# Performance work log

Hardware: AMD Instinct MI355X
Metric: run time of the kernel (lower is better)

The kernel has to match this reference:

```python
import jax, jax.numpy as jnp
import numpy as np

H, I, C, B, T = 128, 270, 3, 1024, 270


def setup_inputs() -> dict:
    key = jax.random.key(0)
    ks = jax.random.split(key, 6)
    inp = {
        "x": jax.random.normal(ks[0], (B, T, I), dtype=jnp.float32),
        "Wf": jax.random.normal(ks[1], (H, I + H), dtype=jnp.float32) * 0.01,
        "Wi": jax.random.normal(ks[2], (H, I + H), dtype=jnp.float32) * 0.01,
        "Wc": jax.random.normal(ks[3], (H, I + H), dtype=jnp.float32) * 0.01,
        "Wo": jax.random.normal(ks[4], (H, I + H), dtype=jnp.float32) * 0.01,
        "Wy": jax.random.normal(ks[5], (C, H), dtype=jnp.float32) * 0.01,
        "bf": jnp.zeros((H,), jnp.float32),
        "bi": jnp.zeros((H,), jnp.float32),
        "bc": jnp.zeros((H,), jnp.float32),
        "bo": jnp.zeros((H,), jnp.float32),
        "by": jnp.zeros((C,), jnp.float32),
    }
    return inp


def _lstm_forward(x, Wf, Wi, Wc, Wo, Wy, bf, bi, bc, bo, by):
    # combined = [h_prev, x_t], so W[:, :H] acts on h, W[:, H:] acts on x.
    Wh = jnp.stack([Wf[:, :H], Wi[:, :H], Wc[:, :H], Wo[:, :H]])      # [4,H,H]
    Wx = jnp.stack([Wf[:, H:], Wi[:, H:], Wc[:, H:], Wo[:, H:]])      # [4,H,I]
    b = jnp.stack([bf, bi, bc, bo])                                   # [4,H]
    # Precompute input projections for all timesteps: one big GEMM.
    xp = jnp.einsum('bti,ghi->tbgh', x, Wx)                           # [T,B,4,H]

    def step(carry, xpt):
        h, c = carry
        pre = xpt + jnp.einsum('bh,gkh->bgk', h, Wh) + b              # [B,4,H]
        f = jax.nn.sigmoid(pre[:, 0])
        i = jax.nn.sigmoid(pre[:, 1])
        g = jnp.tanh(pre[:, 2])
        o = jax.nn.sigmoid(pre[:, 3])
        c_new = f * c + i * g
        h_new = o * jnp.tanh(c_new)
        return (h_new, c_new), h_new

    h0 = jnp.zeros((x.shape[0], H), x.dtype)
    c0 = jnp.zeros((x.shape[0], H), x.dtype)
    _, hs = jax.lax.scan(step, (h0, c0), xp)                          # hs: [T,B,H]
    all_hiddens = jnp.transpose(hs, (1, 0, 2))                        # [B,T,H]
    logits = jnp.einsum('bth,ch->btc', all_hiddens, Wy) + by
    all_outputs = jax.nn.softmax(logits, axis=-1)                     # [B,T,C]
    return all_hiddens, all_outputs


def reference(x, Wf, Wi, Wc, Wo, Wy, bf, bi, bc, bo, by):
    return _lstm_forward(x, Wf, Wi, Wc, Wo, Wy, bf, bi, bc, bo, by)
```

## Files before the change

### kernel.cpp

```cpp
#include <hip/hip_runtime.h>
#include <stdint.h>


typedef __attribute__((ext_vector_type(8))) short short8;
typedef __attribute__((ext_vector_type(4))) float f32x4;
typedef __attribute__((ext_vector_type(2))) float f32x2;
typedef __attribute__((ext_vector_type(4))) unsigned int uint4v;
typedef __attribute__((ext_vector_type(2))) unsigned int u32x2;
typedef unsigned short ush;

__device__ __forceinline__ ush f2bf(float f) {
    unsigned u = __float_as_uint(f);
    return (ush)((u + 0x7FFFu + ((u >> 16) & 1u)) >> 16);
}
__device__ __forceinline__ float bf2f(ush s) { return __uint_as_float(((unsigned)s) << 16); }
__device__ __forceinline__ float sigm_f(float x) {
    x = fminf(fmaxf(x, -30.f), 30.f);
    return __builtin_amdgcn_rcpf(1.f + __expf(-x));
}
__device__ __forceinline__ float tanh_f(float x) {
    x = fminf(fmaxf(x, -15.f), 15.f);
    float e = __expf(-2.f * x);
    return (1.f - e) * __builtin_amdgcn_rcpf(1.f + e);
}
__device__ __forceinline__ void lds_barrier() {
    asm volatile("s_waitcnt lgkmcnt(0)" ::: "memory");
    __builtin_amdgcn_s_barrier();
    __builtin_amdgcn_sched_barrier(0);
    asm volatile("" ::: "memory");
}

__global__ __launch_bounds__(256) void pack_w(
    const float* __restrict__ Wf, const float* __restrict__ Wi,
    const float* __restrict__ Wc, const float* __restrict__ Wo,
    const float* __restrict__ bf_, const float* __restrict__ bi_,
    const float* __restrict__ bc_, const float* __restrict__ bo_,
    ush* __restrict__ Wxp, ush* __restrict__ Whp, float* __restrict__ bpk)
{
    int idx = blockIdx.x * 256 + threadIdx.x;
    if (idx < 512 * 288) {
        int u = idx / 288, i = idx - u * 288;
        int g = u >> 7, j = u & 127;
        const float* Wg = (g == 0) ? Wf : (g == 1) ? Wi : (g == 2) ? Wc : Wo;
        float v = (i < 270) ? Wg[(size_t)j * 398 + 128 + i] : 0.f;
        Wxp[idx] = f2bf(v);
    }
    if (idx < 512 * 128) {
        int u = idx >> 7, k = idx & 127;
        int g = u >> 7, j = u & 127;
        const float* Wg = (g == 0) ? Wf : (g == 1) ? Wi : (g == 2) ? Wc : Wo;
        Whp[idx] = f2bf(Wg[(size_t)j * 398 + k]);
    }
    if (idx < 512) {
        int g = idx >> 7, j = idx & 127;
        const float* bg = (g == 0) ? bf_ : (g == 1) ? bi_ : (g == 2) ? bc_ : bo_;
        bpk[idx] = bg[j];
    }
}

__global__ __launch_bounds__(256, 2) void xp_gemm(
    const float* __restrict__ x, const ush* __restrict__ Wxp,
    const float* __restrict__ bpk, ush* __restrict__ xpc, int t0)
{
    __shared__ ush A_lds[64 * 296];
    const int tid = threadIdx.x;
    const int l = tid & 63, w = tid >> 6;
    const int l16 = l & 15, lq = l >> 4;
    const size_t row0 = (size_t)blockIdx.x * 64;

    const int srow = tid >> 2, sgrp = tid & 3;
    const int r = (int)row0 + srow;
    const int b = r & 1023, tt = (r >> 10) + t0;
    const float* xrow = x + ((size_t)b * 270 + tt) * 270;
    f32x2 stg[9][4];
    #pragma unroll
    for (int ks = 0; ks < 9; ++ks) {
        const int col = ks * 32 + sgrp * 8;
        const float* p = xrow + col;
        if (col + 8 <= 270) {
            stg[ks][0] = *(const f32x2*)p;       stg[ks][1] = *(const f32x2*)(p + 2);
            stg[ks][2] = *(const f32x2*)(p + 4); stg[ks][3] = *(const f32x2*)(p + 6);
        } else {
            float tv[8];
            #pragma unroll
            for (int j = 0; j < 8; ++j) tv[j] = (col + j < 270) ? p[j] : 0.f;
            stg[ks][0] = (f32x2){tv[0], tv[1]}; stg[ks][1] = (f32x2){tv[2], tv[3]};
            stg[ks][2] = (f32x2){tv[4], tv[5]}; stg[ks][3] = (f32x2){tv[6], tv[7]};
        }
    }

    const ush* bptr = Wxp + ((size_t)(w * 128 + l16)) * 288 + lq * 8;
    short8 bA[8], bB[8];
    #pragma unroll
    for (int nt = 0; nt < 8; ++nt) bA[nt] = *(const short8*)(bptr + nt * 4608);
    float bias_v[8];
    #pragma unroll
    for (int nt = 0; nt < 8; ++nt) bias_v[nt] = bpk[w * 128 + nt * 16 + l16];

    {
        ush* wrow = &A_lds[srow * 296 + sgrp * 8];
        #pragma unroll
        for (int ks = 0; ks < 9; ++ks) {
            uint4v o;
            #pragma unroll
            for (int p2 = 0; p2 < 4; ++p2) {
                unsigned v;
                asm("v_cvt_pk_bf16_f32 %0, %1, %2"
                    : "=v"(v) : "v"(stg[ks][p2].x), "v"(stg[ks][p2].y));
                o[p2] = v;
            }
            *(uint4v*)(wrow + ks * 32) = o;
        }
    }
    lds_barrier();

    f32x4 acc[4][8];
    #pragma unroll
    for (int mt = 0; mt < 4; ++mt)
        #pragma unroll
        for (int nt = 0; nt < 8; ++nt)
            acc[mt][nt] = (f32x4){bias_v[nt], bias_v[nt], bias_v[nt], bias_v[nt]};

    #pragma unroll
    for (int ks = 0; ks < 9; ++ks) {
        short8* cur = (ks & 1) ? bB : bA;
        short8* nxt = (ks & 1) ? bA : bB;
        if (ks + 1 < 9) {
            const ush* np = bptr + (ks + 1) * 32;
            #pragma unroll
            for (int nt = 0; nt < 8; ++nt) nxt[nt] = *(const short8*)(np + nt * 4608);
        }
        short8 afr[4];
        #pragma unroll
        for (int mt = 0; mt < 4; ++mt)
            afr[mt] = *(const short8*)(&A_lds[(mt * 16 + l16) * 296 + ks * 32 + lq * 8]);
        #pragma unroll
        for (int mt = 0; mt < 4; ++mt)
            #pragma unroll
            for (int nt = 0; nt < 8; ++nt)
                acc[mt][nt] = __builtin_amdgcn_mfma_f32_16x16x32_bf16(
                    afr[mt], cur[nt], acc[mt][nt], 0, 0, 0);
    }

    const int tloc = (int)(row0 >> 10);
    const int bg0 = ((int)row0 & 1023) >> 4;
    #pragma unroll
    for (int mt = 0; mt < 4; ++mt)
        #pragma unroll
        for (int nt = 0; nt < 8; ++nt) {
            int u = w * 128 + nt * 16 + l16;
            ush* dst = xpc + ((size_t)(tloc * 64 + bg0 + mt) * 512 + u) * 16 + lq * 4;
            #pragma unroll
            for (int q = 0; q < 4; ++q) dst[q] = f2bf(acc[mt][nt][q]);
        }
}

#define STEPB(T, PS)                                                            \
  {                                                                             \
    const int t_ = (T);                                                         \
    short8 afr[4];                                                              \
    _Pragma("unroll") for (int kf = 0; kf < 4; ++kf) {                          \
      int off_ = ((l16 * 128 + kf * 32 + lq * 8) * 2) ^ ((l16 & 7) << 4);       \
      afr[kf] = *(const short8*)((const char*)&h_lds[0][0] + cur * 4096 + off_);\
    }                                                                           \
    f32x4 a0_[4], a1_[4];                                                       \
    _Pragma("unroll") for (int g = 0; g < 4; ++g) {                             \
      a0_[g] = (f32x4){0.f, 0.f, 0.f, 0.f};                                     \
      a1_[g] = (f32x4){0.f, 0.f, 0.f, 0.f};                                     \
    }                                                                           \
    _Pragma("unroll") for (int g = 0; g < 4; ++g) {                             \
      a0_[g] = __builtin_amdgcn_mfma_f32_16x16x32_bf16(afr[0], whf[g][0], a0_[g], 0, 0, 0); \
      a1_[g] = __builtin_amdgcn_mfma_f32_16x16x32_bf16(afr[2], whf[g][2], a1_[g], 0, 0, 0); \
      a0_[g] = __builtin_amdgcn_mfma_f32_16x16x32_bf16(afr[1], whf[g][1], a0_[g], 0, 0, 0); \
      a1_[g] = __builtin_amdgcn_mfma_f32_16x16x32_bf16(afr[3], whf[g][3], a1_[g], 0, 0, 0); \
    }                                                                           \
    f32x4 ay_ = (f32x4){0.f, 0.f, 0.f, 0.f};                                    \
    if (w < 4 && t_ > t0) {               \
      ay_ = __builtin_amdgcn_mfma_f32_16x16x32_bf16(afr[0], wyf[0], ay_, 0, 0, 0); \
      ay_ = __builtin_amdgcn_mfma_f32_16x16x32_bf16(afr[1], wyf[1], ay_, 0, 0, 0); \
      ay_ = __builtin_amdgcn_mfma_f32_16x16x32_bf16(afr[2], wyf[2], ay_, 0, 0, 0); \
      ay_ = __builtin_amdgcn_mfma_f32_16x16x32_bf16(afr[3], wyf[3], ay_, 0, 0, 0); \
    }                                                                           \
    float xg_[4][4];                                                            \
    _Pragma("unroll") for (int g = 0; g < 4; ++g) {                             \
      u32x2 pv_ = PS[g];                                                        \
      xg_[g][0] = __uint_as_float(pv_.x << 16);                                 \
      xg_[g][1] = __uint_as_float(pv_.x & 0xffff0000u);                         \
      xg_[g][2] = __uint_as_float(pv_.y << 16);                                 \
      xg_[g][3] = __uint_as_float(pv_.y & 0xffff0000u);                         \
    }                                                                           \
    if (t_ + 2 < t1) {                                                          \
      const ush* pn_ = xb + (size_t)(t_ + 2 - t0) * TSTEP;                      \
      _Pragma("unroll") for (int g = 0; g < 4; ++g)                             \
        PS[g] = *(const u32x2*)(pn_ + go[g]);                                   \
    }                                                                           \
    float hv_[4];                                                               \
    _Pragma("unroll") for (int q = 0; q < 4; ++q) {                             \
      float pf_ = a0_[0][q] + a1_[0][q] + xg_[0][q];                            \
      float pi_ = a0_[1][q] + a1_[1][q] + xg_[1][q];                            \
      float pc_ = a0_[2][q] + a1_[2][q] + xg_[2][q];                            \
      float po_ = a0_[3][q] + a1_[3][q] + xg_[3][q];                            \
      float fg_ = sigm_f(pf_);                                                  \
      float ig_ = sigm_f(pi_);                                                  \
      float gg_ = tanh_f(pc_);                                                  \
      float og_ = sigm_f(po_);                                                  \
      float cn_ = fg_ * c[q] + ig_ * gg_;                                       \
      c[q] = cn_;                                                               \
      hv_[q] = og_ * tanh_f(cn_);                                               \
    }                                                                           \
    _Pragma("unroll") for (int q = 0; q < 4; ++q) {                             \
      int rr_ = lq * 4 + q;                                                     \
      int off_ = ((rr_ * 128 + jcol) * 2) ^ ((rr_ & 7) << 4);                   \
      *(ush*)((char*)&h_lds[0][0] + (cur ^ 1) * 4096 + off_) = f2bf(hv_[q]);    \
      out0[(size_t)(b0 + rr_) * (270 * 128) + (size_t)t_ * 128 + jcol] = hv_[q];\
    }                                                                           \
    if (w < 4 && t_ > t0) {                                                     \
      float L_ = ((w == 0) ? ay_[0] : (w == 1) ? ay_[1] : (w == 2) ? ay_[2] : ay_[3]) + byl; \
      if (l16 >= 3) L_ = -1e30f;                                                \
      float m_ = fmaxf(L_, __shfl_xor(L_, 1));                                  \
      m_ = fmaxf(m_, __shfl_xor(m_, 2));                                        \
      float e_ = (l16 < 3) ? __expf(L_ - m_) : 0.f;                             \
      float s_ = e_ + __shfl_xor(e_, 1);                                        \
      s_ = s_ + __shfl_xor(s_, 2);                                              \
      if (l16 < 3)                                                              \
        out1[((size_t)(b0 + lq * 4 + w) * 270 + (t_ - 1)) * 3 + l16] = e_ * __builtin_amdgcn_rcpf(s_); \
    }                                                                           \
    lds_barrier();                                                              \
    cur ^= 1;                                                                   \
  }

__global__ __launch_bounds__(512) void lstm_scan(
    const ush* __restrict__ xpc, const ush* __restrict__ Whp,
    float* __restrict__ c_state, float* __restrict__ out0, float* __restrict__ out1,
    const float* __restrict__ Wy, const float* __restrict__ by, int t0, int t1)
{
    __shared__ ush h_lds[2][16 * 128];
    const int tid = threadIdx.x;
    const int l = tid & 63, w = tid >> 6;
    const int l16 = l & 15, lq = l >> 4;
    const int b0 = blockIdx.x * 16;
    const int jcol = w * 16 + l16;

    short8 whf[4][4];
    #pragma unroll
    for (int g = 0; g < 4; ++g) {
        const ush* bw = Whp + ((size_t)(g * 128 + jcol)) * 128 + lq * 8;
        #pragma unroll
        for (int kf = 0; kf < 4; ++kf) whf[g][kf] = *(const short8*)(bw + kf * 32);
    }
    short8 wyf[4];
    #pragma unroll
    for (int kf = 0; kf < 4; ++kf) {
        short8 fr;
        #pragma unroll
        for (int j = 0; j < 8; ++j)
            fr[j] = (l16 < 3) ? (short)f2bf(Wy[l16 * 128 + kf * 32 + lq * 8 + j]) : (short)0;
        wyf[kf] = fr;
    }
    const float byl = (l16 < 3) ? by[l16] : 0.f;

    {
        ush* hp = &h_lds[0][0];
        for (int idx = tid; idx < 2 * 16 * 128; idx += 512) hp[idx] = 0;
    }
    __syncthreads();

    int cur = 0;
    float c[4] = {0.f, 0.f, 0.f, 0.f};
    if (t0 != 0) {
        #pragma unroll
        for (int q = 0; q < 4; ++q)
            c[q] = c_state[(size_t)(b0 + lq * 4 + q) * 128 + jcol];
        for (int idx = tid; idx < 2048; idx += 512) {
            int rr = idx >> 7, k = idx & 127;
            float hvv = out0[(size_t)(b0 + rr) * (270 * 128) + (size_t)(t0 - 1) * 128 + k];
            int off = ((rr * 128 + k) * 2) ^ ((rr & 7) << 4);
            *(ush*)((char*)&h_lds[0][0] + off) = f2bf(hvv);
        }
        __syncthreads();
    }

    const size_t TSTEP = (size_t)64 * 512 * 16;
    const ush* xb = xpc + (size_t)blockIdx.x * 8192;
    int go[4];
    #pragma unroll
    for (int g = 0; g < 4; ++g) go[g] = (g * 128 + jcol) * 16 + lq * 4;

    u32x2 Pa[4], Pb[4];
    #pragma unroll
    for (int g = 0; g < 4; ++g) Pa[g] = *(const u32x2*)(xb + go[g]);
    #pragma unroll
    for (int g = 0; g < 4; ++g) Pb[g] = *(const u32x2*)(xb + TSTEP + go[g]);

    for (int t = t0; t < t1; t += 2) {
        STEPB(t, Pa)
        STEPB(t + 1, Pb)
    }

    {
        short8 afr[4];
        #pragma unroll
        for (int kf = 0; kf < 4; ++kf) {
            int off = ((l16 * 128 + kf * 32 + lq * 8) * 2) ^ ((l16 & 7) << 4);
            afr[kf] = *(const short8*)((const char*)&h_lds[0][0] + cur * 4096 + off);
        }
        if (w < 4) {
            f32x4 ay = (f32x4){0.f, 0.f, 0.f, 0.f};
            ay = __builtin_amdgcn_mfma_f32_16x16x32_bf16(afr[0], wyf[0], ay, 0, 0, 0);
            ay = __builtin_amdgcn_mfma_f32_16x16x32_bf16(afr[1], wyf[1], ay, 0, 0, 0);
            ay = __builtin_amdgcn_mfma_f32_16x16x32_bf16(afr[2], wyf[2], ay, 0, 0, 0);
            ay = __builtin_amdgcn_mfma_f32_16x16x32_bf16(afr[3], wyf[3], ay, 0, 0, 0);
            float L = ((w == 0) ? ay[0] : (w == 1) ? ay[1] : (w == 2) ? ay[2] : ay[3]) + byl;
            if (l16 >= 3) L = -1e30f;
            float m = fmaxf(L, __shfl_xor(L, 1));
            m = fmaxf(m, __shfl_xor(m, 2));
            float e = (l16 < 3) ? __expf(L - m) : 0.f;
            float s = e + __shfl_xor(e, 1);
            s = s + __shfl_xor(s, 2);
            if (l16 < 3)
                out1[((size_t)(b0 + lq * 4 + w) * 270 + (t1 - 1)) * 3 + l16] =
                    e * __builtin_amdgcn_rcpf(s);
        }
    }

    if (t1 != 270) {
        #pragma unroll
        for (int q = 0; q < 4; ++q)
            c_state[(size_t)(b0 + lq * 4 + q) * 128 + jcol] = c[q];
    }
}

extern "C" void kernel_launch(void* const* d_in, const int* in_sizes, int n_in,
                              void* d_out, int out_size, void* d_ws, size_t ws_size,
                              hipStream_t stream) {
    (void)in_sizes; (void)n_in; (void)out_size;
    const float* x   = (const float*)d_in[0];
    const float* Wf  = (const float*)d_in[1];
    const float* Wi  = (const float*)d_in[2];
    const float* Wc  = (const float*)d_in[3];
    const float* Wo  = (const float*)d_in[4];
    const float* Wy  = (const float*)d_in[5];
    const float* bfp = (const float*)d_in[6];
    const float* bip = (const float*)d_in[7];
    const float* bcp = (const float*)d_in[8];
    const float* bop = (const float*)d_in[9];
    const float* byp = (const float*)d_in[10];

    float* out0 = (float*)d_out;
    float* out1 = out0 + (size_t)1024 * 270 * 128;

    long tc = 6;
    {
        const long cand[6] = {270, 90, 54, 30, 18, 6};
        for (int i = 0; i < 6; ++i) {
            size_t need = (size_t)cand[i] * 1048576u + (2u << 20);
            if (need <= ws_size) { tc = cand[i]; break; }
        }
    }
    char* wsb = (char*)d_ws;
    ush* xpc = (ush*)wsb;
    char* fx = wsb + (size_t)tc * 1048576u;
    float* c_state = (float*)fx;
    ush* Wxp = (ush*)(fx + 524288);
    ush* Whp = (ush*)(fx + 524288 + 294912);
    float* bpk = (float*)(fx + 524288 + 294912 + 131072);

    pack_w<<<576, 256, 0, stream>>>(Wf, Wi, Wc, Wo, bfp, bip, bcp, bop, Wxp, Whp, bpk);

    for (int t0 = 0; t0 < 270; t0 += (int)tc) {
        int Tcur = (270 - t0) < (int)tc ? (270 - t0) : (int)tc;
        int rows = Tcur * 1024;
        xp_gemm<<<rows / 64, 256, 0, stream>>>(x, Wxp, bpk, xpc, t0);
        lstm_scan<<<64, 512, 0, stream>>>(xpc, Whp, c_state, out0, out1, Wy, byp,
                                          t0, t0 + Tcur);
    }
}
```

Measured before the change: 501.5 us.

## Fuse input-projection GEMM and recurrent scan into one kernel with double-buffered chunks

Replaces the separate xp_gemm and lstm_scan launches with a single fused kernel. Blocks 0-63 run the recurrent scan on chunk ci-1 while blocks 64-255 compute the input projection for chunk ci into a second buffer, so the GEMM overlaps the latency-bound scan. The chunk size is capped at 54 timesteps. The x-projection is also folded into the MFMA accumulator init instead of being added after the matmuls. The cost is that the GEMM blocks now compete with the scan blocks for CU and memory resources, plus the overhead of more launches.

```diff
diff --git a/kernel.cpp b/kernel.cpp
--- a/kernel.cpp
+++ b/kernel.cpp
@@ -5,7 +5,6 @@
 typedef __attribute__((ext_vector_type(8))) short short8;
 typedef __attribute__((ext_vector_type(4))) float f32x4;
 typedef __attribute__((ext_vector_type(2))) float f32x2;
-typedef __attribute__((ext_vector_type(4))) unsigned int uint4v;
 typedef __attribute__((ext_vector_type(2))) unsigned int u32x2;
 typedef unsigned short ush;
 
@@ -58,128 +57,13 @@
     }
 }
 
-__global__ __launch_bounds__(256, 2) void xp_gemm(
-    const float* __restrict__ x, const ush* __restrict__ Wxp,
-    const float* __restrict__ bpk, ush* __restrict__ xpc, int t0)
-{
-    __shared__ ush A_lds[64 * 296];
-    const int tid = threadIdx.x;
-    const int l = tid & 63, w = tid >> 6;
-    const int l16 = l & 15, lq = l >> 4;
-    const size_t row0 = (size_t)blockIdx.x * 64;
-
-    const int srow = tid >> 2, sgrp = tid & 3;
-    const int r = (int)row0 + srow;
-    const int b = r & 1023, tt = (r >> 10) + t0;
-    const float* xrow = x + ((size_t)b * 270 + tt) * 270;
-    f32x2 stg[9][4];
-    #pragma unroll
-    for (int ks = 0; ks < 9; ++ks) {
-        const int col = ks * 32 + sgrp * 8;
-        const float* p = xrow + col;
-        if (col + 8 <= 270) {
-            stg[ks][0] = *(const f32x2*)p;       stg[ks][1] = *(const f32x2*)(p + 2);
-            stg[ks][2] = *(const f32x2*)(p + 4); stg[ks][3] = *(const f32x2*)(p + 6);
-        } else {
-            float tv[8];
-            #pragma unroll
-            for (int j = 0; j < 8; ++j) tv[j] = (col + j < 270) ? p[j] : 0.f;
-            stg[ks][0] = (f32x2){tv[0], tv[1]}; stg[ks][1] = (f32x2){tv[2], tv[3]};
-            stg[ks][2] = (f32x2){tv[4], tv[5]}; stg[ks][3] = (f32x2){tv[6], tv[7]};
-        }
-    }
-
-    const ush* bptr = Wxp + ((size_t)(w * 128 + l16)) * 288 + lq * 8;
-    short8 bA[8], bB[8];
-    #pragma unroll
-    for (int nt = 0; nt < 8; ++nt) bA[nt] = *(const short8*)(bptr + nt * 4608);
-    float bias_v[8];
-    #pragma unroll
-    for (int nt = 0; nt < 8; ++nt) bias_v[nt] = bpk[w * 128 + nt * 16 + l16];
-
-    {
-        ush* wrow = &A_lds[srow * 296 + sgrp * 8];
-        #pragma unroll
-        for (int ks = 0; ks < 9; ++ks) {
-            uint4v o;
-            #pragma unroll
-            for (int p2 = 0; p2 < 4; ++p2) {
-                unsigned v;
-                asm("v_cvt_pk_bf16_f32 %0, %1, %2"
-                    : "=v"(v) : "v"(stg[ks][p2].x), "v"(stg[ks][p2].y));
-                o[p2] = v;
-            }
-            *(uint4v*)(wrow + ks * 32) = o;
-        }
-    }
-    lds_barrier();
-
-    f32x4 acc[4][8];
-    #pragma unroll
-    for (int mt = 0; mt < 4; ++mt)
-        #pragma unroll
-        for (int nt = 0; nt < 8; ++nt)
-            acc[mt][nt] = (f32x4){bias_v[nt], bias_v[nt], bias_v[nt], bias_v[nt]};
-
-    #pragma unroll
-    for (int ks = 0; ks < 9; ++ks) {
-        short8* cur = (ks & 1) ? bB : bA;
-        short8* nxt = (ks & 1) ? bA : bB;
-        if (ks + 1 < 9) {
-            const ush* np = bptr + (ks + 1) * 32;
-            #pragma unroll
-            for (int nt = 0; nt < 8; ++nt) nxt[nt] = *(const short8*)(np + nt * 4608);
-        }
-        short8 afr[4];
-        #pragma unroll
-        for (int mt = 0; mt < 4; ++mt)
-            afr[mt] = *(const short8*)(&A_lds[(mt * 16 + l16) * 296 + ks * 32 + lq * 8]);
-        #pragma unroll
-        for (int mt = 0; mt < 4; ++mt)
-            #pragma unroll
-            for (int nt = 0; nt < 8; ++nt)
-                acc[mt][nt] = __builtin_amdgcn_mfma_f32_16x16x32_bf16(
-                    afr[mt], cur[nt], acc[mt][nt], 0, 0, 0);
-    }
-
-    const int tloc = (int)(row0 >> 10);
-    const int bg0 = ((int)row0 & 1023) >> 4;
-    #pragma unroll
-    for (int mt = 0; mt < 4; ++mt)
-        #pragma unroll
-        for (int nt = 0; nt < 8; ++nt) {
-            int u = w * 128 + nt * 16 + l16;
-            ush* dst = xpc + ((size_t)(tloc * 64 + bg0 + mt) * 512 + u) * 16 + lq * 4;
-            #pragma unroll
-            for (int q = 0; q < 4; ++q) dst[q] = f2bf(acc[mt][nt][q]);
-        }
-}
-
 #define STEPB(T, PS)                                                            \
   {                                                                             \
     const int t_ = (T);                                                         \
     short8 afr[4];                                                              \
     _Pragma("unroll") for (int kf = 0; kf < 4; ++kf) {                          \
       int off_ = ((l16 * 128 + kf * 32 + lq * 8) * 2) ^ ((l16 & 7) << 4);       \
-      afr[kf] = *(const short8*)((const char*)&h_lds[0][0] + cur * 4096 + off_);\
-    }                                                                           \
-    f32x4 a0_[4], a1_[4];                                                       \
-    _Pragma("unroll") for (int g = 0; g < 4; ++g) {                             \
-      a0_[g] = (f32x4){0.f, 0.f, 0.f, 0.f};                                     \
-      a1_[g] = (f32x4){0.f, 0.f, 0.f, 0.f};                                     \
-    }                                                                           \
-    _Pragma("unroll") for (int g = 0; g < 4; ++g) {                             \
-      a0_[g] = __builtin_amdgcn_mfma_f32_16x16x32_bf16(afr[0], whf[g][0], a0_[g], 0, 0, 0); \
-      a1_[g] = __builtin_amdgcn_mfma_f32_16x16x32_bf16(afr[2], whf[g][2], a1_[g], 0, 0, 0); \
-      a0_[g] = __builtin_amdgcn_mfma_f32_16x16x32_bf16(afr[1], whf[g][1], a0_[g], 0, 0, 0); \
-      a1_[g] = __builtin_amdgcn_mfma_f32_16x16x32_bf16(afr[3], whf[g][3], a1_[g], 0, 0, 0); \
-    }                                                                           \
-    f32x4 ay_ = (f32x4){0.f, 0.f, 0.f, 0.f};                                    \
-    if (w < 4 && t_ > t0) {               \
-      ay_ = __builtin_amdgcn_mfma_f32_16x16x32_bf16(afr[0], wyf[0], ay_, 0, 0, 0); \
-      ay_ = __builtin_amdgcn_mfma_f32_16x16x32_bf16(afr[1], wyf[1], ay_, 0, 0, 0); \
-      ay_ = __builtin_amdgcn_mfma_f32_16x16x32_bf16(afr[2], wyf[2], ay_, 0, 0, 0); \
-      ay_ = __builtin_amdgcn_mfma_f32_16x16x32_bf16(afr[3], wyf[3], ay_, 0, 0, 0); \
+      afr[kf] = *(const short8*)(hbase + cur * 4096 + off_);                    \
     }                                                                           \
     float xg_[4][4];                                                            \
     _Pragma("unroll") for (int g = 0; g < 4; ++g) {                             \
@@ -194,12 +78,30 @@
       _Pragma("unroll") for (int g = 0; g < 4; ++g)                             \
         PS[g] = *(const u32x2*)(pn_ + go[g]);                                   \
     }                                                                           \
+    f32x4 a0_[4], a1_[4];                                                       \
+    _Pragma("unroll") for (int g = 0; g < 4; ++g) {                             \
+      a0_[g] = (f32x4){xg_[g][0], xg_[g][1], xg_[g][2], xg_[g][3]};             \
+      a1_[g] = (f32x4){0.f, 0.f, 0.f, 0.f};                                     \
+    }                                                                           \
+    _Pragma("unroll") for (int g = 0; g < 4; ++g) {                             \
+      a0_[g] = __builtin_amdgcn_mfma_f32_16x16x32_bf16(afr[0], whf[g][0], a0_[g], 0, 0, 0); \
+      a1_[g] = __builtin_amdgcn_mfma_f32_16x16x32_bf16(afr[2], whf[g][2], a1_[g], 0, 0, 0); \
+      a0_[g] = __builtin_amdgcn_mfma_f32_16x16x32_bf16(afr[1], whf[g][1], a0_[g], 0, 0, 0); \
+      a1_[g] = __builtin_amdgcn_mfma_f32_16x16x32_bf16(afr[3], whf[g][3], a1_[g], 0, 0, 0); \
+    }                                                                           \
+    f32x4 ay_ = (f32x4){0.f, 0.f, 0.f, 0.f};                                    \
+    if (w < 4 && t_ > t0) {               \
+      ay_ = __builtin_amdgcn_mfma_f32_16x16x32_bf16(afr[0], wyf[0], ay_, 0, 0, 0); \
+      ay_ = __builtin_amdgcn_mfma_f32_16x16x32_bf16(afr[1], wyf[1], ay_, 0, 0, 0); \
+      ay_ = __builtin_amdgcn_mfma_f32_16x16x32_bf16(afr[2], wyf[2], ay_, 0, 0, 0); \
+      ay_ = __builtin_amdgcn_mfma_f32_16x16x32_bf16(afr[3], wyf[3], ay_, 0, 0, 0); \
+    }                                                                           \
     float hv_[4];                                                               \
     _Pragma("unroll") for (int q = 0; q < 4; ++q) {                             \
-      float pf_ = a0_[0][q] + a1_[0][q] + xg_[0][q];                            \
-      float pi_ = a0_[1][q] + a1_[1][q] + xg_[1][q];                            \
-      float pc_ = a0_[2][q] + a1_[2][q] + xg_[2][q];                            \
-      float po_ = a0_[3][q] + a1_[3][q] + xg_[3][q];                            \
+      float pf_ = a0_[0][q] + a1_[0][q];                                        \
+      float pi_ = a0_[1][q] + a1_[1][q];                                        \
+      float pc_ = a0_[2][q] + a1_[2][q];                                        \
+      float po_ = a0_[3][q] + a1_[3][q];                                        \
       float fg_ = sigm_f(pf_);                                                  \
       float ig_ = sigm_f(pi_);                                                  \
       float gg_ = tanh_f(pc_);                                                  \
@@ -211,7 +113,7 @@
     _Pragma("unroll") for (int q = 0; q < 4; ++q) {                             \
       int rr_ = lq * 4 + q;                                                     \
       int off_ = ((rr_ * 128 + jcol) * 2) ^ ((rr_ & 7) << 4);                   \
-      *(ush*)((char*)&h_lds[0][0] + (cur ^ 1) * 4096 + off_) = f2bf(hv_[q]);    \
+      *(ush*)(hbase + (cur ^ 1) * 4096 + off_) = f2bf(hv_[q]);                  \
       out0[(size_t)(b0 + rr_) * (270 * 128) + (size_t)t_ * 128 + jcol] = hv_[q];\
     }                                                                           \
     if (w < 4 && t_ > t0) {                                                     \
@@ -229,104 +131,195 @@
     cur ^= 1;                                                                   \
   }
 
-__global__ __launch_bounds__(512) void lstm_scan(
-    const ush* __restrict__ xpc, const ush* __restrict__ Whp,
+__global__ __launch_bounds__(512) void fused_step(
+    const float* __restrict__ x, const ush* __restrict__ Wxp,
+    const float* __restrict__ bpk, ush* __restrict__ xpo,
+    const ush* __restrict__ xpi, const ush* __restrict__ Whp,
     float* __restrict__ c_state, float* __restrict__ out0, float* __restrict__ out1,
-    const float* __restrict__ Wy, const float* __restrict__ by, int t0, int t1)
+    const float* __restrict__ Wy, const float* __restrict__ by,
+    int tg0, int grows, int t0, int t1)
 {
-    __shared__ ush h_lds[2][16 * 128];
+    __shared__ ush smem[64 * 296];
     const int tid = threadIdx.x;
     const int l = tid & 63, w = tid >> 6;
     const int l16 = l & 15, lq = l >> 4;
-    const int b0 = blockIdx.x * 16;
-    const int jcol = w * 16 + l16;
-
-    short8 whf[4][4];
+
+    if (blockIdx.x < 64) {
+        if (t1 <= t0) return;
+        char* hbase = (char*)smem;
+        const int b0 = blockIdx.x * 16;
+        const int jcol = w * 16 + l16;
+
+        short8 whf[4][4];
+        #pragma unroll
+        for (int g = 0; g < 4; ++g) {
+            const ush* bw = Whp + ((size_t)(g * 128 + jcol)) * 128 + lq * 8;
+            #pragma unroll
+            for (int kf = 0; kf < 4; ++kf) whf[g][kf] = *(const short8*)(bw + kf * 32);
+        }
+        short8 wyf[4];
+        #pragma unroll
+        for (int kf = 0; kf < 4; ++kf) {
+            short8 fr;
+            #pragma unroll
+            for (int j = 0; j < 8; ++j)
+                fr[j] = (l16 < 3) ? (short)f2bf(Wy[l16 * 128 + kf * 32 + lq * 8 + j]) : (short)0;
+            wyf[kf] = fr;
+        }
+        const float byl = (l16 < 3) ? by[l16] : 0.f;
+
+        for (int idx = tid; idx < 4096; idx += 512) smem[idx] = 0;
+        __syncthreads();
+
+        int cur = 0;
+        float c[4] = {0.f, 0.f, 0.f, 0.f};
+        if (t0 != 0) {
+            #pragma unroll
+            for (int q = 0; q < 4; ++q)
+                c[q] = c_state[(size_t)(b0 + lq * 4 + q) * 128 + jcol];
+            for (int idx = tid; idx < 2048; idx += 512) {
+                int rr = idx >> 7, k = idx & 127;
+                float hvv = out0[(size_t)(b0 + rr) * (270 * 128) + (size_t)(t0 - 1) * 128 + k];
+                int off = ((rr * 128 + k) * 2) ^ ((rr & 7) << 4);
+                *(ush*)(hbase + off) = f2bf(hvv);
+            }
+            __syncthreads();
+        }
+
+        const size_t TSTEP = (size_t)64 * 512 * 16;
+        const ush* xb = xpi + (size_t)blockIdx.x * 8192;
+        int go[4];
+        #pragma unroll
+        for (int g = 0; g < 4; ++g) go[g] = (g * 128 + jcol) * 16 + lq * 4;
+
+        u32x2 Pa[4], Pb[4];
+        #pragma unroll
+        for (int g = 0; g < 4; ++g) Pa[g] = *(const u32x2*)(xb + go[g]);
+        #pragma unroll
+        for (int g = 0; g < 4; ++g) Pb[g] = *(const u32x2*)(xb + TSTEP + go[g]);
+
+        for (int t = t0; t < t1; t += 2) {
+            STEPB(t, Pa)
+            STEPB(t + 1, Pb)
+        }
+
+        {
+            short8 afr[4];
+            #pragma unroll
+            for (int kf = 0; kf < 4; ++kf) {
+                int off = ((l16 * 128 + kf * 32 + lq * 8) * 2) ^ ((l16 & 7) << 4);
+                afr[kf] = *(const short8*)(hbase + cur * 4096 + off);
+            }
+            if (w < 4) {
+                f32x4 ay = (f32x4){0.f, 0.f, 0.f, 0.f};
+                ay = __builtin_amdgcn_mfma_f32_16x16x32_bf16(afr[0], wyf[0], ay, 0, 0, 0);
+                ay = __builtin_amdgcn_mfma_f32_16x16x32_bf16(afr[1], wyf[1], ay, 0, 0, 0);
+                ay = __builtin_amdgcn_mfma_f32_16x16x32_bf16(afr[2], wyf[2], ay, 0, 0, 0);
+                ay = __builtin_amdgcn_mfma_f32_16x16x32_bf16(afr[3], wyf[3], ay, 0, 0, 0);
+                float L = ((w == 0) ? ay[0] : (w == 1) ? ay[1] : (w == 2) ? ay[2] : ay[3]) + byl;
+                if (l16 >= 3) L = -1e30f;
+                float m = fmaxf(L, __shfl_xor(L, 1));
+                m = fmaxf(m, __shfl_xor(m, 2));
+                float e = (l16 < 3) ? __expf(L - m) : 0.f;
+                float s = e + __shfl_xor(e, 1);
+                s = s + __shfl_xor(s, 2);
+                if (l16 < 3)
+                    out1[((size_t)(b0 + lq * 4 + w) * 270 + (t1 - 1)) * 3 + l16] =
+                        e * __builtin_amdgcn_rcpf(s);
+            }
+        }
+        if (t1 != 270) {
+            #pragma unroll
+            for (int q = 0; q < 4; ++q)
+                c_state[(size_t)(b0 + lq * 4 + q) * 128 + jcol] = c[q];
+        }
+        return;
+    }
+
+    if (grows <= 0) return;
+    const int ntiles = grows >> 6;
+    const int wave_m = w >> 2, wave_n = w & 3;
+    const int srow = tid >> 3, cg = tid & 7;
+
+    const ush* bptr = Wxp + ((size_t)(wave_n * 128 + l16)) * 288 + lq * 8;
+    float bias_v[8];
     #pragma unroll
-    for (int g = 0; g < 4; ++g) {
-        const ush* bw = Whp + ((size_t)(g * 128 + jcol)) * 128 + lq * 8;
-        #pragma unroll
-        for (int kf = 0; kf < 4; ++kf) whf[g][kf] = *(const short8*)(bw + kf * 32);
-    }
-    short8 wyf[4];
-    #pragma unroll
-    for (int kf = 0; kf < 4; ++kf) {
-        short8 fr;
-        #pragma unroll
-        for (int j = 0; j < 8; ++j)
-            fr[j] = (l16 < 3) ? (short)f2bf(Wy[l16 * 128 + kf * 32 + lq * 8 + j]) : (short)0;
-        wyf[kf] = fr;
-    }
-    const float byl = (l16 < 3) ? by[l16] : 0.f;
-
-    {
-        ush* hp = &h_lds[0][0];
-        for (int idx = tid; idx < 2 * 16 * 128; idx += 512) hp[idx] = 0;
-    }
-    __syncthreads();
-
-    int cur = 0;
-    float c[4] = {0.f, 0.f, 0.f, 0.f};
-    if (t0 != 0) {
-        #pragma unroll
-        for (int q = 0; q < 4; ++q)
-            c[q] = c_state[(size_t)(b0 + lq * 4 + q) * 128 + jcol];
-        for (int idx = tid; idx < 2048; idx += 512) {
-            int rr = idx >> 7, k = idx & 127;
-            float hvv = out0[(size_t)(b0 + rr) * (270 * 128) + (size_t)(t0 - 1) * 128 + k];
-            int off = ((rr * 128 + k) * 2) ^ ((rr & 7) << 4);
-            *(ush*)((char*)&h_lds[0][0] + off) = f2bf(hvv);
-        }
-        __syncthreads();
-    }
-
-    const size_t TSTEP = (size_t)64 * 512 * 16;
-    const ush* xb = xpc + (size_t)blockIdx.x * 8192;
-    int go[4];
-    #pragma unroll
-    for (int g = 0; g < 4; ++g) go[g] = (g * 128 + jcol) * 16 + lq * 4;
-
-    u32x2 Pa[4], Pb[4];
-    #pragma unroll
-    for (int g = 0; g < 4; ++g) Pa[g] = *(const u32x2*)(xb + go[g]);
-    #pragma unroll
-    for (int g = 0; g < 4; ++g) Pb[g] = *(const u32x2*)(xb + TSTEP + go[g]);
-
-    for (int t = t0; t < t1; t += 2) {
-        STEPB(t, Pa)
-        STEPB(t + 1, Pb)
-    }
-
-    {
-        short8 afr[4];
-        #pragma unroll
-        for (int kf = 0; kf < 4; ++kf) {
-            int off = ((l16 * 128 + kf * 32 + lq * 8) * 2) ^ ((l16 & 7) << 4);
-            afr[kf] = *(const short8*)((const char*)&h_lds[0][0] + cur * 4096 + off);
-        }
-        if (w < 4) {
-            f32x4 ay = (f32x4){0.f, 0.f, 0.f, 0.f};
-            ay = __builtin_amdgcn_mfma_f32_16x16x32_bf16(afr[0], wyf[0], ay, 0, 0, 0);
-            ay = __builtin_amdgcn_mfma_f32_16x16x32_bf16(afr[1], wyf[1], ay, 0, 0, 0);
-            ay = __builtin_amdgcn_mfma_f32_16x16x32_bf16(afr[2], wyf[2], ay, 0, 0, 0);
-            ay = __builtin_amdgcn_mfma_f32_16x16x32_bf16(afr[3], wyf[3], ay, 0, 0, 0);
-            float L = ((w == 0) ? ay[0] : (w == 1) ? ay[1] : (w == 2) ? ay[2] : ay[3]) + byl;
-            if (l16 >= 3) L = -1e30f;
-            float m = fmaxf(L, __shfl_xor(L, 1));
-            m = fmaxf(m, __shfl_xor(m, 2));
-            float e = (l16 < 3) ? __expf(L - m) : 0.f;
-            float s = e + __shfl_xor(e, 1);
-            s = s + __shfl_xor(s, 2);
-            if (l16 < 3)
-                out1[((size_t)(b0 + lq * 4 + w) * 270 + (t1 - 1)) * 3 + l16] =
-                    e * __builtin_amdgcn_rcpf(s);
-        }
-    }
-
-    if (t1 != 270) {
-        #pragma unroll
-        for (int q = 0; q < 4; ++q)
-            c_state[(size_t)(b0 + lq * 4 + q) * 128 + jcol] = c[q];
+    for (int nt = 0; nt < 8; ++nt) bias_v[nt] = bpk[wave_n * 128 + nt * 16 + l16];
+
+    for (int tile = (int)blockIdx.x - 64; tile < ntiles; tile += 192) {
+        const int r = tile * 64 + srow;
+        const int b = r & 1023, tt = (r >> 10) + tg0;
+        const float* xrow = x + ((size_t)b * 270 + tt) * 270;
+        f32x4 stg[9];
+        #pragma unroll
+        for (int ks = 0; ks < 9; ++ks) {
+            const int col = ks * 32 + cg * 4;
+            if (ks < 8) {
+                stg[ks] = *(const f32x4*)(xrow + col);
+            } else {
+                float tv[4];
+                #pragma unroll
+                for (int j = 0; j < 4; ++j) tv[j] = (col + j < 270) ? xrow[col + j] : 0.f;
+                stg[8] = (f32x4){tv[0], tv[1], tv[2], tv[3]};
+            }
+        }
+        lds_barrier();
+        {
+            ush* wp = smem + srow * 296 + cg * 4;
+            #pragma unroll
+            for (int ks = 0; ks < 9; ++ks) {
+                unsigned v0, v1;
+                asm("v_cvt_pk_bf16_f32 %0, %1, %2" : "=v"(v0) : "v"(stg[ks].x), "v"(stg[ks].y));
+                asm("v_cvt_pk_bf16_f32 %0, %1, %2" : "=v"(v1) : "v"(stg[ks].z), "v"(stg[ks].w));
+                u32x2 pk; pk.x = v0; pk.y = v1;
+                *(u32x2*)(wp + ks * 32) = pk;
+            }
+        }
+        short8 bA[8], bB[8];
+        #pragma unroll
+        for (int nt = 0; nt < 8; ++nt) bA[nt] = *(const short8*)(bptr + nt * 4608);
+        lds_barrier();
+
+        f32x4 acc[2][8];
+        #pragma unroll
+        for (int mt = 0; mt < 2; ++mt)
+            #pragma unroll
+            for (int nt = 0; nt < 8; ++nt)
+                acc[mt][nt] = (f32x4){bias_v[nt], bias_v[nt], bias_v[nt], bias_v[nt]};
+
+        #pragma unroll
+        for (int ks = 0; ks < 9; ++ks) {
+            short8* curb = (ks & 1) ? bB : bA;
+            short8* nxtb = (ks & 1) ? bA : bB;
+            if (ks + 1 < 9) {
+                const ush* np = bptr + (ks + 1) * 32;
+                #pragma unroll
+                for (int nt = 0; nt < 8; ++nt) nxtb[nt] = *(const short8*)(np + nt * 4608);
+            }
+            short8 afr[2];
+            #pragma unroll
+            for (int mt = 0; mt < 2; ++mt)
+                afr[mt] = *(const short8*)(&smem[(wave_m * 32 + mt * 16 + l16) * 296 + ks * 32 + lq * 8]);
+            #pragma unroll
+            for (int mt = 0; mt < 2; ++mt)
+                #pragma unroll
+                for (int nt = 0; nt < 8; ++nt)
+                    acc[mt][nt] = __builtin_amdgcn_mfma_f32_16x16x32_bf16(
+                        afr[mt], curb[nt], acc[mt][nt], 0, 0, 0);
+        }
+
+        const int tloc = (tile * 64) >> 10;
+        const int bgrp0 = ((tile * 64) & 1023) >> 4;
+        #pragma unroll
+        for (int mt = 0; mt < 2; ++mt)
+            #pragma unroll
+            for (int nt = 0; nt < 8; ++nt) {
+                const int bgrp = bgrp0 + wave_m * 2 + mt;
+                const int u = wave_n * 128 + nt * 16 + l16;
+                ush* dst = xpo + ((size_t)(tloc * 64 + bgrp) * 512 + u) * 16 + lq * 4;
+                #pragma unroll
+                for (int q = 0; q < 4; ++q) dst[q] = f2bf(acc[mt][nt][q]);
+            }
     }
 }
 
@@ -351,15 +344,17 @@
 
     long tc = 6;
     {
-        const long cand[6] = {270, 90, 54, 30, 18, 6};
-        for (int i = 0; i < 6; ++i) {
-            size_t need = (size_t)cand[i] * 1048576u + (2u << 20);
+        const long cand[4] = {54, 30, 18, 6};
+        for (int i = 0; i < 4; ++i) {
+            size_t need = (size_t)cand[i] * 2097152u + (2u << 20);
             if (need <= ws_size) { tc = cand[i]; break; }
         }
     }
+    const int nch = (int)(270 / tc);
     char* wsb = (char*)d_ws;
-    ush* xpc = (ush*)wsb;
-    char* fx = wsb + (size_t)tc * 1048576u;
+    ush* xpcA = (ush*)wsb;
+    ush* xpcB = (ush*)(wsb + (size_t)tc * 1048576u);
+    char* fx = wsb + (size_t)tc * 2097152u;
     float* c_state = (float*)fx;
     ush* Wxp = (ush*)(fx + 524288);
     ush* Whp = (ush*)(fx + 524288 + 294912);
@@ -367,11 +362,15 @@
 
     pack_w<<<576, 256, 0, stream>>>(Wf, Wi, Wc, Wo, bfp, bip, bcp, bop, Wxp, Whp, bpk);
 
-    for (int t0 = 0; t0 < 270; t0 += (int)tc) {
-        int Tcur = (270 - t0) < (int)tc ? (270 - t0) : (int)tc;
-        int rows = Tcur * 1024;
-        xp_gemm<<<rows / 64, 256, 0, stream>>>(x, Wxp, bpk, xpc, t0);
-        lstm_scan<<<64, 512, 0, stream>>>(xpc, Whp, c_state, out0, out1, Wy, byp,
-                                          t0, t0 + Tcur);
-    }
-}
+    for (int ci = 0; ci <= nch; ++ci) {
+        int g_t0 = ci * (int)tc;
+        int g_rows = (ci < nch) ? (int)tc * 1024 : 0;
+        int s_t0 = (ci > 0) ? (ci - 1) * (int)tc : 0;
+        int s_t1 = (ci > 0) ? ci * (int)tc : 0;
+        ush* xo = (ci & 1) ? xpcB : xpcA;
+        ush* xi = (ci & 1) ? xpcA : xpcB;
+        fused_step<<<256, 512, 0, stream>>>(x, Wxp, bpk, xo, xi, Whp, c_state,
+                                            out0, out1, Wy, byp,
+                                            g_t0, g_rows, s_t0, s_t1);
+    }
+}
```

Measured after the change: 626.7 us, median of 2. 25.0% more time.

## Fold x-projection into MFMA accumulators, merge gate reciprocals, move softmax after barrier

Applied to the files above, without the earlier changes.

The bf16 input projection now seeds the MFMA accumulator, so the separate per-gate add is gone. The sigmoid and tanh gate math is rewritten algebraically to share one reciprocal for the cell update and one for the hidden output, which cuts the number of transcendental and rcp ops on the serial per-step path. The output-softmax MFMA and its epilogue alternate between wave halves on even and odd steps and run after the LDS barrier, taking them off the critical path before the barrier. The combined-denominator form and the tighter clamps may change numerics slightly, including overflow behaviour of the product of denominators.

```diff
diff --git a/kernel.cpp b/kernel.cpp
--- a/kernel.cpp
+++ b/kernel.cpp
@@ -14,15 +14,6 @@
     return (ush)((u + 0x7FFFu + ((u >> 16) & 1u)) >> 16);
 }
 __device__ __forceinline__ float bf2f(ush s) { return __uint_as_float(((unsigned)s) << 16); }
-__device__ __forceinline__ float sigm_f(float x) {
-    x = fminf(fmaxf(x, -30.f), 30.f);
-    return __builtin_amdgcn_rcpf(1.f + __expf(-x));
-}
-__device__ __forceinline__ float tanh_f(float x) {
-    x = fminf(fmaxf(x, -15.f), 15.f);
-    float e = __expf(-2.f * x);
-    return (1.f - e) * __builtin_amdgcn_rcpf(1.f + e);
-}
 __device__ __forceinline__ void lds_barrier() {
     asm volatile("s_waitcnt lgkmcnt(0)" ::: "memory");
     __builtin_amdgcn_s_barrier();
@@ -158,28 +149,11 @@
 #define STEPB(T, PS)                                                            \
   {                                                                             \
     const int t_ = (T);                                                         \
+    const bool lw_ = (((w >> 2) ^ (t_ & 1)) == 0) && (t_ > t0);                 \
     short8 afr[4];                                                              \
     _Pragma("unroll") for (int kf = 0; kf < 4; ++kf) {                          \
       int off_ = ((l16 * 128 + kf * 32 + lq * 8) * 2) ^ ((l16 & 7) << 4);       \
-      afr[kf] = *(const short8*)((const char*)&h_lds[0][0] + cur * 4096 + off_);\
-    }                                                                           \
-    f32x4 a0_[4], a1_[4];                                                       \
-    _Pragma("unroll") for (int g = 0; g < 4; ++g) {                             \
-      a0_[g] = (f32x4){0.f, 0.f, 0.f, 0.f};                                     \
-      a1_[g] = (f32x4){0.f, 0.f, 0.f, 0.f};                                     \
-    }                                                                           \
-    _Pragma("unroll") for (int g = 0; g < 4; ++g) {                             \
-      a0_[g] = __builtin_amdgcn_mfma_f32_16x16x32_bf16(afr[0], whf[g][0], a0_[g], 0, 0, 0); \
-      a1_[g] = __builtin_amdgcn_mfma_f32_16x16x32_bf16(afr[2], whf[g][2], a1_[g], 0, 0, 0); \
-      a0_[g] = __builtin_amdgcn_mfma_f32_16x16x32_bf16(afr[1], whf[g][1], a0_[g], 0, 0, 0); \
-      a1_[g] = __builtin_amdgcn_mfma_f32_16x16x32_bf16(afr[3], whf[g][3], a1_[g], 0, 0, 0); \
-    }                                                                           \
-    f32x4 ay_ = (f32x4){0.f, 0.f, 0.f, 0.f};                                    \
-    if (w < 4 && t_ > t0) {               \
-      ay_ = __builtin_amdgcn_mfma_f32_16x16x32_bf16(afr[0], wyf[0], ay_, 0, 0, 0); \
-      ay_ = __builtin_amdgcn_mfma_f32_16x16x32_bf16(afr[1], wyf[1], ay_, 0, 0, 0); \
-      ay_ = __builtin_amdgcn_mfma_f32_16x16x32_bf16(afr[2], wyf[2], ay_, 0, 0, 0); \
-      ay_ = __builtin_amdgcn_mfma_f32_16x16x32_bf16(afr[3], wyf[3], ay_, 0, 0, 0); \
+      afr[kf] = *(const short8*)(hbase + cur * 4096 + off_);                    \
     }                                                                           \
     float xg_[4][4];                                                            \
     _Pragma("unroll") for (int g = 0; g < 4; ++g) {                             \
@@ -194,28 +168,56 @@
       _Pragma("unroll") for (int g = 0; g < 4; ++g)                             \
         PS[g] = *(const u32x2*)(pn_ + go[g]);                                   \
     }                                                                           \
+    f32x4 a0_[4], a1_[4];                                                       \
+    _Pragma("unroll") for (int g = 0; g < 4; ++g) {                             \
+      a0_[g] = (f32x4){xg_[g][0], xg_[g][1], xg_[g][2], xg_[g][3]};             \
+      a1_[g] = (f32x4){0.f, 0.f, 0.f, 0.f};                                     \
+    }                                                                           \
+    _Pragma("unroll") for (int g = 0; g < 4; ++g) {                             \
+      a0_[g] = __builtin_amdgcn_mfma_f32_16x16x32_bf16(afr[0], whf[g][0], a0_[g], 0, 0, 0); \
+      a1_[g] = __builtin_amdgcn_mfma_f32_16x16x32_bf16(afr[2], whf[g][2], a1_[g], 0, 0, 0); \
+      a0_[g] = __builtin_amdgcn_mfma_f32_16x16x32_bf16(afr[1], whf[g][1], a0_[g], 0, 0, 0); \
+      a1_[g] = __builtin_amdgcn_mfma_f32_16x16x32_bf16(afr[3], whf[g][3], a1_[g], 0, 0, 0); \
+    }                                                                           \
+    f32x4 ay0_ = (f32x4){0.f, 0.f, 0.f, 0.f};                                   \
+    f32x4 ay1_ = (f32x4){0.f, 0.f, 0.f, 0.f};                                   \
+    if (lw_) {                            \
+      ay0_ = __builtin_amdgcn_mfma_f32_16x16x32_bf16(afr[0], wyf[0], ay0_, 0, 0, 0); \
+      ay1_ = __builtin_amdgcn_mfma_f32_16x16x32_bf16(afr[2], wyf[2], ay1_, 0, 0, 0); \
+      ay0_ = __builtin_amdgcn_mfma_f32_16x16x32_bf16(afr[1], wyf[1], ay0_, 0, 0, 0); \
+      ay1_ = __builtin_amdgcn_mfma_f32_16x16x32_bf16(afr[3], wyf[3], ay1_, 0, 0, 0); \
+    }                                                                           \
     float hv_[4];                                                               \
     _Pragma("unroll") for (int q = 0; q < 4; ++q) {                             \
-      float pf_ = a0_[0][q] + a1_[0][q] + xg_[0][q];                            \
-      float pi_ = a0_[1][q] + a1_[1][q] + xg_[1][q];                            \
-      float pc_ = a0_[2][q] + a1_[2][q] + xg_[2][q];                            \
-      float po_ = a0_[3][q] + a1_[3][q] + xg_[3][q];                            \
-      float fg_ = sigm_f(pf_);                                                  \
-      float ig_ = sigm_f(pi_);                                                  \
-      float gg_ = tanh_f(pc_);                                                  \
-      float og_ = sigm_f(po_);                                                  \
-      float cn_ = fg_ * c[q] + ig_ * gg_;                                       \
+      float pf_ = fminf(fmaxf(a0_[0][q] + a1_[0][q], -20.f), 20.f);             \
+      float pi_ = fminf(fmaxf(a0_[1][q] + a1_[1][q], -20.f), 20.f);             \
+      float pc_ = fminf(fmaxf(a0_[2][q] + a1_[2][q], -10.f), 10.f);             \
+      float po_ = fminf(fmaxf(a0_[3][q] + a1_[3][q], -20.f), 20.f);             \
+      float df_ = 1.f + __expf(-pf_);                                           \
+      float di_ = 1.f + __expf(-pi_);                                           \
+      float ec2_ = __expf(-2.f * pc_);                                          \
+      float dc_ = 1.f + ec2_;                                                   \
+      float do2_ = 1.f + __expf(-po_);                                          \
+      float didc_ = di_ * dc_;                                                  \
+      float num_ = c[q] * didc_ + (1.f - ec2_) * df_;                           \
+      float cn_ = num_ * __builtin_amdgcn_rcpf(df_ * didc_);                    \
       c[q] = cn_;                                                               \
-      hv_[q] = og_ * tanh_f(cn_);                                               \
+      float cnc_ = fminf(fmaxf(cn_, -10.f), 10.f);                              \
+      float et2_ = __expf(-2.f * cnc_);                                         \
+      hv_[q] = (1.f - et2_) * __builtin_amdgcn_rcpf(do2_ * (1.f + et2_));       \
     }                                                                           \
     _Pragma("unroll") for (int q = 0; q < 4; ++q) {                             \
       int rr_ = lq * 4 + q;                                                     \
       int off_ = ((rr_ * 128 + jcol) * 2) ^ ((rr_ & 7) << 4);                   \
-      *(ush*)((char*)&h_lds[0][0] + (cur ^ 1) * 4096 + off_) = f2bf(hv_[q]);    \
+      *(ush*)(hbase + (cur ^ 1) * 4096 + off_) = f2bf(hv_[q]);                  \
       out0[(size_t)(b0 + rr_) * (270 * 128) + (size_t)t_ * 128 + jcol] = hv_[q];\
     }                                                                           \
-    if (w < 4 && t_ > t0) {                                                     \
-      float L_ = ((w == 0) ? ay_[0] : (w == 1) ? ay_[1] : (w == 2) ? ay_[2] : ay_[3]) + byl; \
+    lds_barrier();                                                              \
+       \
+    if (lw_) {                                                                  \
+      f32x4 ay_ = ay0_ + ay1_;                                                  \
+      int ww_ = w & 3;                                                          \
+      float L_ = ((ww_ == 0) ? ay_[0] : (ww_ == 1) ? ay_[1] : (ww_ == 2) ? ay_[2] : ay_[3]) + byl; \
       if (l16 >= 3) L_ = -1e30f;                                                \
       float m_ = fmaxf(L_, __shfl_xor(L_, 1));                                  \
       m_ = fmaxf(m_, __shfl_xor(m_, 2));                                        \
@@ -223,9 +225,8 @@
       float s_ = e_ + __shfl_xor(e_, 1);                                        \
       s_ = s_ + __shfl_xor(s_, 2);                                              \
       if (l16 < 3)                                                              \
-        out1[((size_t)(b0 + lq * 4 + w) * 270 + (t_ - 1)) * 3 + l16] = e_ * __builtin_amdgcn_rcpf(s_); \
-    }                                                                           \
-    lds_barrier();                                                              \
+        out1[((size_t)(b0 + lq * 4 + ww_) * 270 + (t_ - 1)) * 3 + l16] = e_ * __builtin_amdgcn_rcpf(s_); \
+    }                                                                           \
     cur ^= 1;                                                                   \
   }
 
@@ -240,6 +241,7 @@
     const int l16 = l & 15, lq = l >> 4;
     const int b0 = blockIdx.x * 16;
     const int jcol = w * 16 + l16;
+    char* hbase = (char*)&h_lds[0][0];
 
     short8 whf[4][4];
     #pragma unroll
@@ -275,7 +277,7 @@
             int rr = idx >> 7, k = idx & 127;
             float hvv = out0[(size_t)(b0 + rr) * (270 * 128) + (size_t)(t0 - 1) * 128 + k];
             int off = ((rr * 128 + k) * 2) ^ ((rr & 7) << 4);
-            *(ush*)((char*)&h_lds[0][0] + off) = f2bf(hvv);
+            *(ush*)(hbase + off) = f2bf(hvv);
         }
         __syncthreads();
     }
@@ -302,7 +304,7 @@
         #pragma unroll
         for (int kf = 0; kf < 4; ++kf) {
             int off = ((l16 * 128 + kf * 32 + lq * 8) * 2) ^ ((l16 & 7) << 4);
-            afr[kf] = *(const short8*)((const char*)&h_lds[0][0] + cur * 4096 + off);
+            afr[kf] = *(const short8*)(hbase + cur * 4096 + off);
         }
         if (w < 4) {
             f32x4 ay = (f32x4){0.f, 0.f, 0.f, 0.f};
```

Result: faster. 477.4 us (-4.8%).
